# Kernel optimization log

Measured on AMD Instinct MI355X. Metric: run time of the kernel, lower is better.

The kernel has to match this reference:

```python
import jax, jax.numpy as jnp
import numpy as np

H = 16
D_MODEL = 1024
D_K = D_MODEL // H
NEG_INF = -1e9


def setup_inputs() -> dict:
    key = jax.random.key(0)
    ks = jax.random.split(key, 11)
    B, S = 4, 2048
    scale = 1.0 / np.sqrt(D_MODEL)
    inp = {
        "query": jax.random.normal(ks[0], (B, S, D_MODEL), jnp.float32),
        "key": jax.random.normal(ks[1], (B, S, D_MODEL), jnp.float32),
        "value": jax.random.normal(ks[2], (B, S, D_MODEL), jnp.float32),
        "Wq": jax.random.normal(ks[3], (D_MODEL, D_MODEL), jnp.float32) * scale,
        "bq": jnp.zeros((D_MODEL,), jnp.float32),
        "Wk": jax.random.normal(ks[4], (D_MODEL, D_MODEL), jnp.float32) * scale,
        "bk": jnp.zeros((D_MODEL,), jnp.float32),
        "Wv": jax.random.normal(ks[5], (D_MODEL, D_MODEL), jnp.float32) * scale,
        "bv": jnp.zeros((D_MODEL,), jnp.float32),
        "Wo": jax.random.normal(ks[6], (D_MODEL, D_MODEL), jnp.float32) * scale,
        "bo": jnp.zeros((D_MODEL,), jnp.float32),
    }
    return inp


def _split_heads(x):
    # [B, S, D] -> [B, H, S, D_K]
    B, S, _ = x.shape
    return x.reshape(B, S, H, D_K).transpose(0, 2, 1, 3)


def reference(query, key, value, Wq, bq, Wk, bk, Wv, bv, Wo, bo):
    # Linear projections (torch Linear: y = x @ W.T + b)
    q = _split_heads(query @ Wq.T + bq)   # [B,H,S,Dk]
    k = _split_heads(key @ Wk.T + bk)
    v = _split_heads(value @ Wv.T + bv)

    S = q.shape[2]
    scores = jnp.einsum("bhqd,bhkd->bhqk", q, k) / jnp.sqrt(jnp.float32(D_K))
    causal = jnp.tril(jnp.ones((S, S), jnp.bool_))  # [S,S]
    scores = jnp.where(causal[None, None], scores, NEG_INF)
    p_attn = jax.nn.softmax(scores, axis=-1)  # dropout p=0.0 (eval)
    x = jnp.einsum("bhqk,bhkd->bhqd", p_attn, v)  # [B,H,S,Dk]
    B = x.shape[0]
    x = x.transpose(0, 2, 1, 3).reshape(B, S, H * D_K)
    return x @ Wo.T + bo
```

## Files before the change

### kernel.cpp

```cpp
#include <hip/hip_runtime.h>
#include <hip/hip_bf16.h>
#include <stdint.h>

#define NH 16
#define SEQ 2048
#define DMODEL 1024
#define DK 64
#define BATCH 4
#define M_TOT 8192

#define LOG2E 1.44269504088896f
#define QSCALE (0.125f * LOG2E)

typedef short v8bf __attribute__((ext_vector_type(8)));
typedef float f32x4 __attribute__((ext_vector_type(4)));

__device__ __forceinline__ unsigned pack_bf2(float a, float b) {
  union { __hip_bfloat162 h; unsigned u; } v;
  v.h = __float22bfloat162_rn(make_float2(a, b));
  return v.u;
}

__device__ __forceinline__ unsigned short f2bf(float f) {
  union { __hip_bfloat16 h; unsigned short u; } v;
  v.h = __float2bfloat16(f);
  return v.u;
}

__device__ __forceinline__ void async_load16(const void* g, void* l) {
  __builtin_amdgcn_global_load_lds(
      (const __attribute__((address_space(1))) unsigned int*)(uintptr_t)g,
      (__attribute__((address_space(3))) unsigned int*)(unsigned)(uintptr_t)l,
      16, 0, 0);
}

__global__ __launch_bounds__(256)
void cvt_kernel(const float* __restrict__ q, const float* __restrict__ k,
                const float* __restrict__ v,
                const float* __restrict__ wq, const float* __restrict__ wk,
                const float* __restrict__ wv, const float* __restrict__ wo,
                unsigned short* __restrict__ oq, unsigned short* __restrict__ ok,
                unsigned short* __restrict__ ov,
                unsigned short* __restrict__ owq, unsigned short* __restrict__ owk,
                unsigned short* __restrict__ owv, unsigned short* __restrict__ owo)
{
  const size_t XN = (size_t)M_TOT * DMODEL;
  const size_t WN = (size_t)DMODEL * DMODEL;
  const float* s; unsigned short* d; size_t n;
  switch (blockIdx.y) {
    case 0: s = q;  d = oq;  n = XN; break;
    case 1: s = k;  d = ok;  n = XN; break;
    case 2: s = v;  d = ov;  n = XN; break;
    case 3: s = wq; d = owq; n = WN; break;
    case 4: s = wk; d = owk; n = WN; break;
    case 5: s = wv; d = owv; n = WN; break;
    default: s = wo; d = owo; n = WN; break;
  }
  for (size_t i = ((size_t)blockIdx.x * 256 + threadIdx.x) * 8; i < n;
       i += (size_t)gridDim.x * 256 * 8) {
    float4 a = *(const float4*)(s + i);
    float4 b = *(const float4*)(s + i + 4);
    uint4 p = { pack_bf2(a.x, a.y), pack_bf2(a.z, a.w),
                pack_bf2(b.x, b.y), pack_bf2(b.z, b.w) };
    *(uint4*)(d + i) = p;
  }
}

__global__ __launch_bounds__(256, 2)
void proj_bf16_kernel(const unsigned short* __restrict__ Xq,
                      const unsigned short* __restrict__ Xk,
                      const unsigned short* __restrict__ Xv,
                      const unsigned short* __restrict__ Wqc,
                      const unsigned short* __restrict__ Wkc,
                      const unsigned short* __restrict__ Wvc,
                      const float* __restrict__ bq, const float* __restrict__ bk,
                      const float* __restrict__ bv,
                      unsigned short* __restrict__ Qp, unsigned short* __restrict__ Kp,
                      unsigned short* __restrict__ Vp)
{
  const int z = blockIdx.z;
  const unsigned short* A = (z == 0) ? Xq : (z == 1) ? Xk : Xv;
  const unsigned short* W = (z == 0) ? Wqc : (z == 1) ? Wkc : Wvc;
  const float* bias = (z == 0) ? bq : (z == 1) ? bk : bv;
  unsigned short* Out = (z == 0) ? Qp : (z == 1) ? Kp : Vp;
  const float scale = (z == 0) ? QSCALE : 1.0f;

  __shared__ unsigned short As[128 * 64];
  __shared__ unsigned short Bs[128 * 64];

  const int tid  = threadIdx.x;
  const int m0   = blockIdx.x * 128;
  const int n0   = blockIdx.y * 128;
  const int lane = tid & 63;
  const int wave = tid >> 6;
  const int quad = lane >> 4;
  const int l16  = lane & 15;
  const int wm   = (wave >> 1) * 64;
  const int wn   = (wave & 1) * 64;
  const int lrow = lane >> 3;
  const int lcol = lane & 7;

  f32x4 acc[4][4];
#pragma unroll
  for (int i = 0; i < 4; ++i)
#pragma unroll
    for (int j = 0; j < 4; ++j) acc[i][j] = (f32x4){0.f, 0.f, 0.f, 0.f};

  for (int k0 = 0; k0 < DMODEL; k0 += 64) {
#pragma unroll
    for (int i = 0; i < 4; ++i) {
      int row = wave * 32 + i * 8 + lrow;
      int gc = (lcol ^ (row & 7)) * 8;
      async_load16(A + (size_t)(m0 + row) * DMODEL + k0 + gc, &As[(wave * 32 + i * 8) * 64]);
      async_load16(W + (size_t)(n0 + row) * DMODEL + k0 + gc, &Bs[(wave * 32 + i * 8) * 64]);
    }
    __syncthreads();

#pragma unroll
    for (int ks = 0; ks < 2; ++ks) {
      v8bf af[4], bf[4];
#pragma unroll
      for (int i = 0; i < 4; ++i)
        af[i] = *(const v8bf*)&As[(wm + i * 16 + l16) * 64 + ((ks * 4 + quad) ^ (l16 & 7)) * 8];
#pragma unroll
      for (int j = 0; j < 4; ++j)
        bf[j] = *(const v8bf*)&Bs[(wn + j * 16 + l16) * 64 + ((ks * 4 + quad) ^ (l16 & 7)) * 8];
#pragma unroll
      for (int i = 0; i < 4; ++i)
#pragma unroll
        for (int j = 0; j < 4; ++j)
          acc[i][j] = __builtin_amdgcn_mfma_f32_16x16x32_bf16(af[i], bf[j], acc[i][j], 0, 0, 0);
    }
    __syncthreads();
  }

  if (z < 2) {
#pragma unroll
    for (int j = 0; j < 4; ++j) {
      int colg = n0 + wn + j * 16 + l16;
      float bj = bias[colg];
      int h = colg >> 6, d = colg & 63;
#pragma unroll
      for (int i = 0; i < 4; ++i) {
#pragma unroll
        for (int reg = 0; reg < 4; ++reg) {
          int mrow = m0 + wm + i * 16 + quad * 4 + reg;
          int bb = mrow >> 11, ss = mrow & 2047;
          float val = (acc[i][j][reg] + bj) * scale;
          Out[(((size_t)bb * NH + h) * SEQ + ss) * DK + d] = f2bf(val);
        }
      }
    }
  } else {
#pragma unroll
    for (int j = 0; j < 4; ++j) {
      int colg = n0 + wn + j * 16 + l16;
      float bj = bias[colg];
      int h = colg >> 6, d = colg & 63;
#pragma unroll
      for (int i = 0; i < 4; ++i) {
        int mrow = m0 + wm + i * 16 + quad * 4;
        int bb = mrow >> 11, ss = mrow & 2047;
        uint2 pk = { pack_bf2(acc[i][j][0] + bj, acc[i][j][1] + bj),
                     pack_bf2(acc[i][j][2] + bj, acc[i][j][3] + bj) };
        *(uint2*)(Out + (((size_t)bb * NH + h) * DK + d) * SEQ + ss) = pk;
      }
    }
  }
}

__global__ __launch_bounds__(256, 2)
void attn_kernel(const unsigned short* __restrict__ Qp,
                 const unsigned short* __restrict__ Kp,
                 const unsigned short* __restrict__ VTp,
                 unsigned short* __restrict__ Xout)
{
  const int y  = blockIdx.y;
  const int r  = y & 3, jj = y >> 2;
  const int qt = (jj == 0) ? (15 - r) : (jj == 1) ? (8 + r) : (jj == 2) ? (7 - r) : r;
  const int bh = blockIdx.x;
  const int b  = bh >> 4, h = bh & 15;

  const unsigned short* Qb = Qp  + ((size_t)bh * SEQ + qt * 128) * DK;
  const unsigned short* Kb = Kp  + (size_t)bh * SEQ * DK;
  const unsigned short* Vb = VTp + (size_t)bh * DK * SEQ;

  __shared__ unsigned short Ks[2][64 * 64];
  __shared__ unsigned short VTs[2][64 * 64];
  __shared__ unsigned short Ps[4][16 * 64];

  const int tid  = threadIdx.x;
  const int lane = tid & 63, wave = tid >> 6;
  const int quad = lane >> 4, l16 = lane & 15;
  const int row_lo = qt * 128 + wave * 32;

  v8bf qf[2][2];
#pragma unroll
  for (int rf = 0; rf < 2; ++rf)
#pragma unroll
    for (int ks = 0; ks < 2; ++ks)
      qf[rf][ks] = *(const v8bf*)(Qb + (size_t)(wave * 32 + rf * 16 + l16) * DK + ks * 32 + quad * 8);

  float lp[2][4];
  f32x4 o[2][4];
#pragma unroll
  for (int rf = 0; rf < 2; ++rf)
#pragma unroll
    for (int reg = 0; reg < 4; ++reg) lp[rf][reg] = 0.f;
#pragma unroll
  for (int rf = 0; rf < 2; ++rf)
#pragma unroll
    for (int df = 0; df < 4; ++df) o[rf][df] = (f32x4){0.f, 0.f, 0.f, 0.f};

  const int nchunk = 2 * (qt + 1);
  const int lrow = lane >> 3;
  const int lcol = lane & 7;

#pragma unroll
  for (int is = 0; is < 2; ++is) {
    int row = wave * 16 + is * 8 + lrow;
    int cK = ((lcol ^ (row & 7)) * 8);
    async_load16(Kb + (size_t)row * DK + cK, &Ks[0][(wave * 16 + is * 8) * 64]);
    async_load16(Vb + (size_t)row * SEQ + cK, &VTs[0][(wave * 16 + is * 8) * 64]);
  }
  __syncthreads();

  for (int c = 0; c < nchunk; ++c) {
    const int buf = c & 1;
    const int kb  = c * 64;

    if (c + 1 < nchunk) {
      const int kb2 = kb + 64;
#pragma unroll
      for (int is = 0; is < 2; ++is) {
        int row = wave * 16 + is * 8 + lrow;
        int cc = ((lcol ^ (row & 7)) * 8);
        async_load16(Kb + (size_t)(kb2 + row) * DK + cc, &Ks[buf ^ 1][(wave * 16 + is * 8) * 64]);
        async_load16(Vb + (size_t)row * SEQ + kb2 + cc, &VTs[buf ^ 1][(wave * 16 + is * 8) * 64]);
      }
    }

    if (kb <= row_lo + 31) {
      f32x4 s[2][4];
#pragma unroll
      for (int rf = 0; rf < 2; ++rf)
#pragma unroll
        for (int nf = 0; nf < 4; ++nf) s[rf][nf] = (f32x4){0.f, 0.f, 0.f, 0.f};
      __builtin_amdgcn_s_setprio(1);
#pragma unroll
      for (int ks = 0; ks < 2; ++ks)
#pragma unroll
        for (int nf = 0; nf < 4; ++nf) {
          v8bf kf = *(const v8bf*)&Ks[buf][(nf * 16 + l16) * 64 + ((ks * 4 + quad) ^ (l16 & 7)) * 8];
          s[0][nf] = __builtin_amdgcn_mfma_f32_16x16x32_bf16(qf[0][ks], kf, s[0][nf], 0, 0, 0);
          s[1][nf] = __builtin_amdgcn_mfma_f32_16x16x32_bf16(qf[1][ks], kf, s[1][nf], 0, 0, 0);
        }
      __builtin_amdgcn_s_setprio(0);

      if (kb + 63 > row_lo) {
#pragma unroll
        for (int rf = 0; rf < 2; ++rf)
#pragma unroll
          for (int nf = 0; nf < 4; ++nf) {
            int col = kb + nf * 16 + l16;
#pragma unroll
            for (int reg = 0; reg < 4; ++reg)
              if (col > row_lo + rf * 16 + quad * 4 + reg) s[rf][nf][reg] = -1e30f;
          }
      }

#pragma unroll
      for (int rf = 0; rf < 2; ++rf) {
#pragma unroll
        for (int nf = 0; nf < 4; ++nf)
#pragma unroll
          for (int reg = 0; reg < 4; ++reg)
            s[rf][nf][reg] = __builtin_amdgcn_exp2f(s[rf][nf][reg]);
#pragma unroll
        for (int reg = 0; reg < 4; ++reg)
          lp[rf][reg] += (s[rf][0][reg] + s[rf][1][reg]) + (s[rf][2][reg] + s[rf][3][reg]);

#pragma unroll
        for (int nf = 0; nf < 4; ++nf)
#pragma unroll
          for (int reg = 0; reg < 4; ++reg)
            Ps[wave][(quad * 4 + reg) * 64 +
                     (((nf * 2 + (l16 >> 3)) ^ (quad * 2)) * 8) + (l16 & 7)] =
                f2bf(s[rf][nf][reg]);

        __builtin_amdgcn_s_setprio(1);
#pragma unroll
        for (int ks = 0; ks < 2; ++ks) {
          v8bf pf = *(const v8bf*)&Ps[wave][l16 * 64 + (((ks * 4 + quad) ^ ((l16 >> 2) * 2)) * 8)];
#pragma unroll
          for (int df = 0; df < 4; ++df) {
            v8bf vf = *(const v8bf*)&VTs[buf][(df * 16 + l16) * 64 + ((ks * 4 + quad) ^ (l16 & 7)) * 8];
            o[rf][df] = __builtin_amdgcn_mfma_f32_16x16x32_bf16(pf, vf, o[rf][df], 0, 0, 0);
          }
        }
        __builtin_amdgcn_s_setprio(0);
      }
    }
    __syncthreads();
  }

#pragma unroll
  for (int rf = 0; rf < 2; ++rf) {
#pragma unroll
    for (int off = 1; off < 16; off <<= 1)
#pragma unroll
      for (int reg = 0; reg < 4; ++reg) lp[rf][reg] += __shfl_xor(lp[rf][reg], off);
    float inv[4];
#pragma unroll
    for (int reg = 0; reg < 4; ++reg) inv[reg] = 1.0f / lp[rf][reg];
#pragma unroll
    for (int df = 0; df < 4; ++df)
#pragma unroll
      for (int reg = 0; reg < 4; ++reg) {
        int qrow = row_lo + rf * 16 + quad * 4 + reg;
        Xout[(size_t)(b * SEQ + qrow) * DMODEL + h * DK + df * 16 + l16] =
            f2bf(o[rf][df][reg] * inv[reg]);
      }
  }
}

__global__ __launch_bounds__(256, 2)
void oproj_kernel(const unsigned short* __restrict__ Xa,
                  const unsigned short* __restrict__ Woc,
                  const float* __restrict__ bo,
                  float* __restrict__ Out)
{
  __shared__ unsigned short As[128 * 64];
  __shared__ unsigned short Bs[128 * 64];

  const int tid  = threadIdx.x;
  const int m0   = blockIdx.x * 128;
  const int n0   = blockIdx.y * 128;
  const int lane = tid & 63;
  const int wave = tid >> 6;
  const int quad = lane >> 4;
  const int l16  = lane & 15;
  const int wm   = (wave >> 1) * 64;
  const int wn   = (wave & 1) * 64;
  const int lrow = lane >> 3;
  const int lcol = lane & 7;

  f32x4 acc[4][4];
#pragma unroll
  for (int i = 0; i < 4; ++i)
#pragma unroll
    for (int j = 0; j < 4; ++j) acc[i][j] = (f32x4){0.f, 0.f, 0.f, 0.f};

  for (int k0 = 0; k0 < DMODEL; k0 += 64) {
#pragma unroll
    for (int i = 0; i < 4; ++i) {
      int row = wave * 32 + i * 8 + lrow;
      int gc = (lcol ^ (row & 7)) * 8;
      async_load16(Xa  + (size_t)(m0 + row) * DMODEL + k0 + gc, &As[(wave * 32 + i * 8) * 64]);
      async_load16(Woc + (size_t)(n0 + row) * DMODEL + k0 + gc, &Bs[(wave * 32 + i * 8) * 64]);
    }
    __syncthreads();

#pragma unroll
    for (int ks = 0; ks < 2; ++ks) {
      v8bf af[4], bf[4];
#pragma unroll
      for (int i = 0; i < 4; ++i)
        af[i] = *(const v8bf*)&As[(wm + i * 16 + l16) * 64 + ((ks * 4 + quad) ^ (l16 & 7)) * 8];
#pragma unroll
      for (int j = 0; j < 4; ++j)
        bf[j] = *(const v8bf*)&Bs[(wn + j * 16 + l16) * 64 + ((ks * 4 + quad) ^ (l16 & 7)) * 8];
#pragma unroll
      for (int i = 0; i < 4; ++i)
#pragma unroll
        for (int j = 0; j < 4; ++j)
          acc[i][j] = __builtin_amdgcn_mfma_f32_16x16x32_bf16(af[i], bf[j], acc[i][j], 0, 0, 0);
    }
    __syncthreads();
  }

#pragma unroll
  for (int j = 0; j < 4; ++j) {
    int colg = n0 + wn + j * 16 + l16;
    float bj = bo[colg];
#pragma unroll
    for (int i = 0; i < 4; ++i) {
#pragma unroll
      for (int reg = 0; reg < 4; ++reg) {
        int mrow = m0 + wm + i * 16 + quad * 4 + reg;
        Out[(size_t)mrow * DMODEL + colg] = acc[i][j][reg] + bj;
      }
    }
  }
}

extern "C" void kernel_launch(void* const* d_in, const int* in_sizes, int n_in,
                              void* d_out, int out_size, void* d_ws, size_t ws_size,
                              hipStream_t stream)
{
  const float* query = (const float*)d_in[0];
  const float* key   = (const float*)d_in[1];
  const float* value = (const float*)d_in[2];
  const float* Wq = (const float*)d_in[3];
  const float* bq = (const float*)d_in[4];
  const float* Wk = (const float*)d_in[5];
  const float* bk = (const float*)d_in[6];
  const float* Wv = (const float*)d_in[7];
  const float* bv = (const float*)d_in[8];
  const float* Wo = (const float*)d_in[9];
  const float* bo = (const float*)d_in[10];

  const size_t tsz = (size_t)M_TOT * DMODEL;
  const size_t wsz = (size_t)DMODEL * DMODEL;
  unsigned short* Qp  = (unsigned short*)d_ws;
  unsigned short* Kp  = Qp + tsz;
  unsigned short* Vp  = Kp + tsz;
  unsigned short* Xa  = Vp + tsz;
  unsigned short* Xqc = Xa + tsz;
  unsigned short* Xkc = Xqc + tsz;
  unsigned short* Xvc = Xkc + tsz;
  unsigned short* Wqc = Xvc + tsz;
  unsigned short* Wkc = Wqc + wsz;
  unsigned short* Wvc = Wkc + wsz;
  unsigned short* Woc = Wvc + wsz;

  cvt_kernel<<<dim3(1024, 7), 256, 0, stream>>>(query, key, value, Wq, Wk, Wv, Wo,
                                                Xqc, Xkc, Xvc, Wqc, Wkc, Wvc, Woc);
  proj_bf16_kernel<<<dim3(64, 8, 3), 256, 0, stream>>>(Xqc, Xkc, Xvc, Wqc, Wkc, Wvc,
                                                       bq, bk, bv, Qp, Kp, Vp);
  attn_kernel<<<dim3(64, 16), 256, 0, stream>>>(Qp, Kp, Vp, Xa);
  oproj_kernel<<<dim3(64, 8), 256, 0, stream>>>(Xa, Woc, bo, (float*)d_out);
}
```

Baseline: 305.4 us.

## Compute transposed score tiles and pass P to PV MFMA via lane shuffles

Swaps the MFMA operand order so score tiles come out transposed (keys along registers, queries along lanes). The P operand for the PV MFMA is then built in registers with bf16 packing and cross-lane shuffles instead of a round trip through per-wave shared memory. The row-sum reduction becomes a per-lane accumulation plus two xor shuffles. This removes the LDS scalar stores and loads for P and the associated LDS traffic, at the cost of 16 ds_bpermute-style shuffles and selects per rf per chunk.

```diff
diff --git a/kernel.cpp b/kernel.cpp
--- a/kernel.cpp
+++ b/kernel.cpp
@@ -187,13 +187,16 @@
 
   __shared__ unsigned short Ks[2][64 * 64];
   __shared__ unsigned short VTs[2][64 * 64];
-  __shared__ unsigned short Ps[4][16 * 64];
 
   const int tid  = threadIdx.x;
   const int lane = tid & 63, wave = tid >> 6;
   const int quad = lane >> 4, l16 = lane & 15;
   const int row_lo = qt * 128 + wave * 32;
 
+  const int laneA = l16 + 16 * ((2 * quad) & 3);
+  const int laneB = l16 + 16 * ((2 * quad + 1) & 3);
+  const bool loq = (quad < 2);
+
   v8bf qf[2][2];
 #pragma unroll
   for (int rf = 0; rf < 2; ++rf)
@@ -201,12 +204,9 @@
     for (int ks = 0; ks < 2; ++ks)
       qf[rf][ks] = *(const v8bf*)(Qb + (size_t)(wave * 32 + rf * 16 + l16) * DK + ks * 32 + quad * 8);
 
-  float lp[2][4];
+  float lp2[2];
   f32x4 o[2][4];
-#pragma unroll
-  for (int rf = 0; rf < 2; ++rf)
-#pragma unroll
-    for (int reg = 0; reg < 4; ++reg) lp[rf][reg] = 0.f;
+  lp2[0] = lp2[1] = 0.f;
 #pragma unroll
   for (int rf = 0; rf < 2; ++rf)
 #pragma unroll
@@ -241,32 +241,34 @@
     }
 
     if (kb <= row_lo + 31) {
-      f32x4 s[2][4];
+      f32x4 s2[2][4];
 #pragma unroll
       for (int rf = 0; rf < 2; ++rf)
 #pragma unroll
-        for (int nf = 0; nf < 4; ++nf) s[rf][nf] = (f32x4){0.f, 0.f, 0.f, 0.f};
+        for (int nf = 0; nf < 4; ++nf) s2[rf][nf] = (f32x4){0.f, 0.f, 0.f, 0.f};
       __builtin_amdgcn_s_setprio(1);
 #pragma unroll
       for (int ks = 0; ks < 2; ++ks)
 #pragma unroll
         for (int nf = 0; nf < 4; ++nf) {
           v8bf kf = *(const v8bf*)&Ks[buf][(nf * 16 + l16) * 64 + ((ks * 4 + quad) ^ (l16 & 7)) * 8];
-          s[0][nf] = __builtin_amdgcn_mfma_f32_16x16x32_bf16(qf[0][ks], kf, s[0][nf], 0, 0, 0);
-          s[1][nf] = __builtin_amdgcn_mfma_f32_16x16x32_bf16(qf[1][ks], kf, s[1][nf], 0, 0, 0);
+          s2[0][nf] = __builtin_amdgcn_mfma_f32_16x16x32_bf16(kf, qf[0][ks], s2[0][nf], 0, 0, 0);
+          s2[1][nf] = __builtin_amdgcn_mfma_f32_16x16x32_bf16(kf, qf[1][ks], s2[1][nf], 0, 0, 0);
         }
       __builtin_amdgcn_s_setprio(0);
 
       if (kb + 63 > row_lo) {
 #pragma unroll
-        for (int rf = 0; rf < 2; ++rf)
+        for (int rf = 0; rf < 2; ++rf) {
+          int qrow = row_lo + rf * 16 + l16;
 #pragma unroll
           for (int nf = 0; nf < 4; ++nf) {
-            int col = kb + nf * 16 + l16;
+            int kcol = kb + nf * 16 + quad * 4;
 #pragma unroll
             for (int reg = 0; reg < 4; ++reg)
-              if (col > row_lo + rf * 16 + quad * 4 + reg) s[rf][nf][reg] = -1e30f;
+              if (kcol + reg > qrow) s2[rf][nf][reg] = -1e30f;
           }
+        }
       }
 
 #pragma unroll
@@ -275,30 +277,36 @@
         for (int nf = 0; nf < 4; ++nf)
 #pragma unroll
           for (int reg = 0; reg < 4; ++reg)
-            s[rf][nf][reg] = __builtin_amdgcn_exp2f(s[rf][nf][reg]);
-#pragma unroll
-        for (int reg = 0; reg < 4; ++reg)
-          lp[rf][reg] += (s[rf][0][reg] + s[rf][1][reg]) + (s[rf][2][reg] + s[rf][3][reg]);
-
+            s2[rf][nf][reg] = __builtin_amdgcn_exp2f(s2[rf][nf][reg]);
 #pragma unroll
         for (int nf = 0; nf < 4; ++nf)
-#pragma unroll
-          for (int reg = 0; reg < 4; ++reg)
-            Ps[wave][(quad * 4 + reg) * 64 +
-                     (((nf * 2 + (l16 >> 3)) ^ (quad * 2)) * 8) + (l16 & 7)] =
-                f2bf(s[rf][nf][reg]);
-
-        __builtin_amdgcn_s_setprio(1);
+          lp2[rf] += (s2[rf][nf][0] + s2[rf][nf][1]) + (s2[rf][nf][2] + s2[rf][nf][3]);
+
+        int w[4][2];
+#pragma unroll
+        for (int nf = 0; nf < 4; ++nf) {
+          w[nf][0] = (int)pack_bf2(s2[rf][nf][0], s2[rf][nf][1]);
+          w[nf][1] = (int)pack_bf2(s2[rf][nf][2], s2[rf][nf][3]);
+        }
+
 #pragma unroll
         for (int ks = 0; ks < 2; ++ks) {
-          v8bf pf = *(const v8bf*)&Ps[wave][l16 * 64 + (((ks * 4 + quad) ^ ((l16 >> 2) * 2)) * 8)];
+          union { int wi[4]; v8bf v; } pf;
+#pragma unroll
+          for (int t = 0; t < 4; ++t) {
+            int srcl = (t < 2) ? laneA : laneB;
+            int r1 = __shfl(w[2 * ks][t & 1], srcl);
+            int r2 = __shfl(w[2 * ks + 1][t & 1], srcl);
+            pf.wi[t] = loq ? r1 : r2;
+          }
+          __builtin_amdgcn_s_setprio(1);
 #pragma unroll
           for (int df = 0; df < 4; ++df) {
             v8bf vf = *(const v8bf*)&VTs[buf][(df * 16 + l16) * 64 + ((ks * 4 + quad) ^ (l16 & 7)) * 8];
-            o[rf][df] = __builtin_amdgcn_mfma_f32_16x16x32_bf16(pf, vf, o[rf][df], 0, 0, 0);
+            o[rf][df] = __builtin_amdgcn_mfma_f32_16x16x32_bf16(pf.v, vf, o[rf][df], 0, 0, 0);
           }
+          __builtin_amdgcn_s_setprio(0);
         }
-        __builtin_amdgcn_s_setprio(0);
       }
     }
     __syncthreads();
@@ -306,20 +314,19 @@
 
 #pragma unroll
   for (int rf = 0; rf < 2; ++rf) {
-#pragma unroll
-    for (int off = 1; off < 16; off <<= 1)
-#pragma unroll
-      for (int reg = 0; reg < 4; ++reg) lp[rf][reg] += __shfl_xor(lp[rf][reg], off);
-    float inv[4];
-#pragma unroll
-    for (int reg = 0; reg < 4; ++reg) inv[reg] = 1.0f / lp[rf][reg];
+    lp2[rf] += __shfl_xor(lp2[rf], 16);
+    lp2[rf] += __shfl_xor(lp2[rf], 32);
+    float inv = 1.0f / lp2[rf];
+    float invd[4];
+#pragma unroll
+    for (int reg = 0; reg < 4; ++reg) invd[reg] = __shfl(inv, quad * 4 + reg);
 #pragma unroll
     for (int df = 0; df < 4; ++df)
 #pragma unroll
       for (int reg = 0; reg < 4; ++reg) {
         int qrow = row_lo + rf * 16 + quad * 4 + reg;
         Xout[(size_t)(b * SEQ + qrow) * DMODEL + h * DK + df * 16 + l16] =
-            f2bf(o[rf][df][reg] * inv[reg]);
+            f2bf(o[rf][df][reg] * invd[reg]);
       }
   }
 }
```

Result: no change. 307.1 us (+0.5%).
